# Optimization experiments

Hardware: AMD Instinct MI355X
Metric: run time of the kernel (lower is better)

## Reference

```python
import jax, jax.numpy as jnp
import numpy as np

N = 100000
IN_DIM = 256
H1 = 128
H2 = 64
E = 3200000


def setup_inputs() -> dict:
    key = jax.random.key(0)
    k1, k2, k3, k4 = jax.random.split(key, 4)
    x = jax.random.normal(k1, (N, IN_DIM), dtype=jnp.float32)
    edge_index = jax.random.randint(k2, (2, E), 0, N, dtype=jnp.int64)
    # GCNConv params (glorot weights, zero bias as in PyG defaults)
    W1 = jax.random.normal(k3, (IN_DIM, H1), dtype=jnp.float32) * (1.0 / np.sqrt(IN_DIM))
    b1 = jnp.zeros((H1,), dtype=jnp.float32)
    W2 = jax.random.normal(k4, (H1, H2), dtype=jnp.float32) * (1.0 / np.sqrt(H1))
    b2 = jnp.zeros((H2,), dtype=jnp.float32)
    return {"x": x, "edge_index": edge_index, "W1": W1, "b1": b1, "W2": W2, "b2": b2}


def _gcn_conv(x, W, b, row, col, norm, n_nodes):
    # PyG GCNConv: y = D^{-1/2} (A+I) D^{-1/2} (x W) + b
    h = x @ W                                   # [N, out]
    msg = h[col] * norm[:, None]                # gather + edge scaling
    agg = jax.ops.segment_sum(msg, row, num_segments=n_nodes)  # scatter-add
    return agg + b


def reference(x, edge_index, W1, b1, W2, b2):
    n_nodes = x.shape[0]
    # add self-loops
    loop = jnp.arange(n_nodes, dtype=edge_index.dtype)
    row = jnp.concatenate([edge_index[0], loop])  # target nodes
    col = jnp.concatenate([edge_index[1], loop])  # source nodes
    # symmetric normalization D^{-1/2} A_hat D^{-1/2}
    deg = jax.ops.segment_sum(jnp.ones_like(row, dtype=x.dtype), row, num_segments=n_nodes)
    dinv = jnp.where(deg > 0, jax.lax.rsqrt(deg), 0.0)
    norm = dinv[row] * dinv[col]                # per-edge coefficient
    h = jax.nn.relu(_gcn_conv(x, W1, b1, row, col, norm, n_nodes))
    z = jax.nn.relu(_gcn_conv(h, W2, b2, row, col, norm, n_nodes))
    return z
```

## Files before the change

### kernel.cpp

```cpp
#include <hip/hip_runtime.h>

constexpr int NN = 100000;
constexpr int NE = 3200000;
constexpr int D0 = 256;
constexpr int D1 = 128;
constexpr int D2 = 64;

constexpr int BSHIFT = 9;
constexpr int NPB = 1 << BSHIFT;
constexpr int NBUCK = (NN + NPB - 1) >> BSHIFT;
constexpr int PBLK = 256;
constexpr int CHUNK = (NE + PBLK - 1) / PBLK;

typedef unsigned short ushort8v __attribute__((ext_vector_type(8)));

static __device__ __forceinline__ float bf2f(unsigned short u) {
  return __uint_as_float(((unsigned)u) << 16);
}
static __device__ __forceinline__ unsigned short f2bf(float x) {
  unsigned u = __float_as_uint(x);
  unsigned r = (u + 0x7FFFu + ((u >> 16) & 1u)) >> 16;
  return (unsigned short)r;
}

__global__ __launch_bounds__(256) void count_bucket_k(const int* __restrict__ rows,
                                                      unsigned* __restrict__ gcnt) {
  __shared__ unsigned hist[NBUCK];
  int tid = threadIdx.x;
  for (int i = tid; i < NBUCK; i += 256) hist[i] = 0;
  __syncthreads();
  int s = blockIdx.x * CHUNK;
  int e = s + CHUNK; if (e > NE) e = NE;
  for (int i = s + tid; i < e; i += 256)
    atomicAdd(&hist[((unsigned)rows[i]) >> BSHIFT], 1u);
  __syncthreads();
  for (int i = tid; i < NBUCK; i += 256)
    if (hist[i]) atomicAdd(&gcnt[i], hist[i]);
}

__global__ __launch_bounds__(256) void bucket_scan_k(const unsigned* __restrict__ gcnt,
                                                     unsigned* __restrict__ boff,
                                                     unsigned* __restrict__ gcursor) {
  __shared__ unsigned s[256];
  int t = threadIdx.x;
  unsigned v = (t < NBUCK) ? gcnt[t] : 0u;
  s[t] = v;
  __syncthreads();
  for (int off = 1; off < 256; off <<= 1) {
    unsigned u = (t >= off) ? s[t - off] : 0u;
    __syncthreads();
    s[t] += u;
    __syncthreads();
  }
  if (t < NBUCK) {
    boff[t + 1] = s[t];
    gcursor[t] = s[t] - v;
  }
  if (t == 0) boff[0] = 0u;
}

__global__ __launch_bounds__(256) void partition_k(const int* __restrict__ rows,
                                                   const int* __restrict__ cols,
                                                   unsigned* __restrict__ gcursor,
                                                   unsigned* __restrict__ bucketed) {
  __shared__ unsigned hist[NBUCK], base[NBUCK];
  int tid = threadIdx.x;
  for (int i = tid; i < NBUCK; i += 256) hist[i] = 0;
  __syncthreads();
  int s = blockIdx.x * CHUNK;
  int e = s + CHUNK; if (e > NE) e = NE;
  for (int i = s + tid; i < e; i += 256)
    atomicAdd(&hist[((unsigned)rows[i]) >> BSHIFT], 1u);
  __syncthreads();
  for (int i = tid; i < NBUCK; i += 256)
    base[i] = hist[i] ? atomicAdd(&gcursor[i], hist[i]) : 0u;
  __syncthreads();
  for (int i = tid; i < NBUCK; i += 256) hist[i] = 0;
  __syncthreads();
  for (int i = s + tid; i < e; i += 256) {
    unsigned r = (unsigned)rows[i];
    unsigned b = r >> BSHIFT;
    unsigned p = ((r & (unsigned)(NPB - 1)) << 17) | (unsigned)cols[i];
    unsigned pos = base[b] + atomicAdd(&hist[b], 1u);
    bucketed[pos] = p;
  }
}

__global__ __launch_bounds__(256) void build_k(const unsigned* __restrict__ bucketed,
                                               const unsigned* __restrict__ boff,
                                               unsigned* __restrict__ row_start,
                                               float* __restrict__ dinv,
                                               int* __restrict__ col_sorted) {
  __shared__ unsigned hist[NPB], sc[NPB], cur[NPB];
  const int b = blockIdx.x, tid = threadIdx.x;
  hist[tid] = 0; hist[tid + 256] = 0;
  __syncthreads();
  const unsigned s0 = boff[b], e0 = boff[b + 1];
  for (unsigned i = s0 + tid; i < e0; i += 256)
    atomicAdd(&hist[bucketed[i] >> 17], 1u);
  __syncthreads();
  sc[tid] = hist[tid]; sc[tid + 256] = hist[tid + 256];
  __syncthreads();
  for (int off = 1; off < NPB; off <<= 1) {
    unsigned v0 = (tid >= off) ? sc[tid - off] : 0u;
    unsigned v1 = (tid + 256 >= off) ? sc[tid + 256 - off] : 0u;
    __syncthreads();
    sc[tid] += v0; sc[tid + 256] += v1;
    __syncthreads();
  }
  cur[tid] = tid ? sc[tid - 1] : 0u;
  cur[tid + 256] = sc[tid + 255];
  for (int idx = tid; idx <= NPB; idx += 256) {
    int node = b * NPB + idx;
    if (node <= NN) {
      unsigned ex = idx ? sc[idx - 1] : 0u;
      row_start[node] = s0 + ex;
      if (idx < NPB && node < NN) dinv[node] = rsqrtf((float)hist[idx] + 1.0f);
    }
  }
  __syncthreads();
  for (unsigned i = s0 + tid; i < e0; i += 256) {
    unsigned p = bucketed[i];
    unsigned pos = s0 + atomicAdd(&cur[p >> 17], 1u);
    col_sorted[pos] = (int)(p & 0x1FFFFu);
  }
}

template <int BM, int BN, int BK, int TM, int TN, int K, bool BF16_OUT>
__global__ __launch_bounds__(256) void gemm_scale_k(const float* __restrict__ A,
                                                    const float* __restrict__ W,
                                                    const float* __restrict__ dinv,
                                                    void* __restrict__ outp, int M) {
  constexpr int TX = BN / TN;
  constexpr int TY = BM / TM;
  static_assert(TX * TY == 256, "thread shape");
  __shared__ float As[BK][BM];
  __shared__ float Ws[BK][BN];
  const int tid = threadIdx.x;
  const int tx = tid % TX, ty = tid / TX;
  const int rowBase = blockIdx.x * BM;

  float acc[TM][TN];
#pragma unroll
  for (int i = 0; i < TM; i++)
#pragma unroll
    for (int j = 0; j < TN; j++) acc[i][j] = 0.f;

  constexpr int AF4 = BM * BK / 4 / 256;
  constexpr int WF4 = BK * BN / 4 / 256;

  for (int k0 = 0; k0 < K; k0 += BK) {
#pragma unroll
    for (int q = 0; q < AF4; q++) {
      int f = tid + q * 256;
      int r = f / (BK / 4);
      int kk = (f % (BK / 4)) * 4;
      float4 v = make_float4(0.f, 0.f, 0.f, 0.f);
      int gr = rowBase + r;
      if (gr < M) v = *(const float4*)&A[(size_t)gr * K + k0 + kk];
      As[kk + 0][r] = v.x;
      As[kk + 1][r] = v.y;
      As[kk + 2][r] = v.z;
      As[kk + 3][r] = v.w;
    }
#pragma unroll
    for (int q = 0; q < WF4; q++) {
      int f = tid + q * 256;
      int kk = f / (BN / 4);
      int c = (f % (BN / 4)) * 4;
      *(float4*)&Ws[kk][c] = *(const float4*)&W[(size_t)(k0 + kk) * BN + c];
    }
    __syncthreads();
#pragma unroll
    for (int kk = 0; kk < BK; kk++) {
      float a[TM], wv[TN];
#pragma unroll
      for (int i = 0; i < TM; i += 4) {
        float4 t = *(const float4*)&As[kk][ty * TM + i];
        a[i] = t.x; a[i + 1] = t.y; a[i + 2] = t.z; a[i + 3] = t.w;
      }
#pragma unroll
      for (int j = 0; j < TN; j += 4) {
        float4 t = *(const float4*)&Ws[kk][tx * TN + j];
        wv[j] = t.x; wv[j + 1] = t.y; wv[j + 2] = t.z; wv[j + 3] = t.w;
      }
#pragma unroll
      for (int i = 0; i < TM; i++)
#pragma unroll
        for (int j = 0; j < TN; j++) acc[i][j] += a[i] * wv[j];
    }
    __syncthreads();
  }

#pragma unroll
  for (int i = 0; i < TM; i++) {
    int gr = rowBase + ty * TM + i;
    if (gr < M) {
      float d = dinv[gr];
      if constexpr (BF16_OUT) {
        unsigned short* out = (unsigned short*)outp;
#pragma unroll
        for (int j = 0; j < TN; j += 4) {
          ushort4 o;
          o.x = f2bf(acc[i][j + 0] * d);
          o.y = f2bf(acc[i][j + 1] * d);
          o.z = f2bf(acc[i][j + 2] * d);
          o.w = f2bf(acc[i][j + 3] * d);
          *(ushort4*)&out[(size_t)gr * BN + tx * TN + j] = o;
        }
      } else {
        float* out = (float*)outp;
#pragma unroll
        for (int j = 0; j < TN; j += 4) {
          float4 o;
          o.x = acc[i][j + 0] * d;
          o.y = acc[i][j + 1] * d;
          o.z = acc[i][j + 2] * d;
          o.w = acc[i][j + 3] * d;
          *(float4*)&out[(size_t)gr * BN + tx * TN + j] = o;
        }
      }
    }
  }
}

__global__ __launch_bounds__(256) void prop1_k(const unsigned short* __restrict__ hp,
                                               const unsigned* __restrict__ row_start,
                                               const int* __restrict__ cols,
                                               const float* __restrict__ dinv,
                                               const float* __restrict__ bias,
                                               float* __restrict__ out) {
  int wid = (blockIdx.x * 256 + threadIdx.x) >> 6;
  int lane = threadIdx.x & 63;
  if (wid >= NN) return;
  const int r = wid;
  const int q = lane >> 4, f = lane & 15;

  float a0[8], a1[8];
#pragma unroll
  for (int k = 0; k < 8; k++) { a0[k] = 0.f; a1[k] = 0.f; }
  if (q == 0) {
    ushort8v v = *(const ushort8v*)(hp + (size_t)r * D1 + f * 8);
#pragma unroll
    for (int k = 0; k < 8; k++) a0[k] = bf2f(v[k]);
  }

  unsigned s = row_start[r], e = row_start[r + 1];
  for (unsigned base = s; base < e; base += 64) {
    int cnt = (int)min(64u, e - base);
    int c = (lane < cnt) ? cols[base + lane] : 0;
    int j = 0;
    for (; j + 8 <= cnt; j += 8) {
      int c0 = __shfl(c, j + q);
      int c1 = __shfl(c, j + 4 + q);
      ushort8v v0 = *(const ushort8v*)(hp + (size_t)c0 * D1 + f * 8);
      ushort8v v1 = *(const ushort8v*)(hp + (size_t)c1 * D1 + f * 8);
#pragma unroll
      for (int k = 0; k < 8; k++) a0[k] += bf2f(v0[k]);
#pragma unroll
      for (int k = 0; k < 8; k++) a1[k] += bf2f(v1[k]);
    }
    for (; j + 4 <= cnt; j += 4) {
      int c0 = __shfl(c, j + q);
      ushort8v v0 = *(const ushort8v*)(hp + (size_t)c0 * D1 + f * 8);
#pragma unroll
      for (int k = 0; k < 8; k++) a0[k] += bf2f(v0[k]);
    }
    if (j < cnt) {
      int c0 = __shfl(c, j + q);
      if (j + q < cnt) {
        ushort8v v0 = *(const ushort8v*)(hp + (size_t)c0 * D1 + f * 8);
#pragma unroll
        for (int k = 0; k < 8; k++) a0[k] += bf2f(v0[k]);
      }
    }
  }

#pragma unroll
  for (int k = 0; k < 8; k++) a0[k] += a1[k];
#pragma unroll
  for (int k = 0; k < 8; k++) a0[k] += __shfl_xor(a0[k], 16);
#pragma unroll
  for (int k = 0; k < 8; k++) a0[k] += __shfl_xor(a0[k], 32);

  if (q == 0) {
    float dr = dinv[r];
    float4 b0 = *(const float4*)&bias[f * 8];
    float4 b1v = *(const float4*)&bias[f * 8 + 4];
    float4 o0, o1;
    o0.x = fmaxf(a0[0] * dr + b0.x, 0.f);
    o0.y = fmaxf(a0[1] * dr + b0.y, 0.f);
    o0.z = fmaxf(a0[2] * dr + b0.z, 0.f);
    o0.w = fmaxf(a0[3] * dr + b0.w, 0.f);
    o1.x = fmaxf(a0[4] * dr + b1v.x, 0.f);
    o1.y = fmaxf(a0[5] * dr + b1v.y, 0.f);
    o1.z = fmaxf(a0[6] * dr + b1v.z, 0.f);
    o1.w = fmaxf(a0[7] * dr + b1v.w, 0.f);
    *(float4*)&out[(size_t)r * D1 + f * 8] = o0;
    *(float4*)&out[(size_t)r * D1 + f * 8 + 4] = o1;
  }
}

__global__ __launch_bounds__(256) void prop2_k(const unsigned short* __restrict__ hp,
                                               const unsigned* __restrict__ row_start,
                                               const int* __restrict__ cols,
                                               const float* __restrict__ dinv,
                                               const float* __restrict__ bias,
                                               float* __restrict__ out) {
  int wid = (blockIdx.x * 256 + threadIdx.x) >> 6;
  int lane = threadIdx.x & 63;
  if (wid >= NN) return;
  const int r = wid;
  const int q = lane >> 3, f = lane & 7;

  float a0[8], a1[8];
#pragma unroll
  for (int k = 0; k < 8; k++) { a0[k] = 0.f; a1[k] = 0.f; }
  if (q == 0) {
    ushort8v v = *(const ushort8v*)(hp + (size_t)r * D2 + f * 8);
#pragma unroll
    for (int k = 0; k < 8; k++) a0[k] = bf2f(v[k]);
  }

  unsigned s = row_start[r], e = row_start[r + 1];
  for (unsigned base = s; base < e; base += 64) {
    int cnt = (int)min(64u, e - base);
    int c = (lane < cnt) ? cols[base + lane] : 0;
    int j = 0;
    for (; j + 16 <= cnt; j += 16) {
      int c0 = __shfl(c, j + q);
      int c1 = __shfl(c, j + 8 + q);
      ushort8v v0 = *(const ushort8v*)(hp + (size_t)c0 * D2 + f * 8);
      ushort8v v1 = *(const ushort8v*)(hp + (size_t)c1 * D2 + f * 8);
#pragma unroll
      for (int k = 0; k < 8; k++) a0[k] += bf2f(v0[k]);
#pragma unroll
      for (int k = 0; k < 8; k++) a1[k] += bf2f(v1[k]);
    }
    for (; j + 8 <= cnt; j += 8) {
      int c0 = __shfl(c, j + q);
      ushort8v v0 = *(const ushort8v*)(hp + (size_t)c0 * D2 + f * 8);
#pragma unroll
      for (int k = 0; k < 8; k++) a0[k] += bf2f(v0[k]);
    }
    if (j < cnt) {
      int c0 = __shfl(c, j + q);
      if (j + q < cnt) {
        ushort8v v0 = *(const ushort8v*)(hp + (size_t)c0 * D2 + f * 8);
#pragma unroll
        for (int k = 0; k < 8; k++) a0[k] += bf2f(v0[k]);
      }
    }
  }

#pragma unroll
  for (int k = 0; k < 8; k++) a0[k] += a1[k];
#pragma unroll
  for (int k = 0; k < 8; k++) a0[k] += __shfl_xor(a0[k], 8);
#pragma unroll
  for (int k = 0; k < 8; k++) a0[k] += __shfl_xor(a0[k], 16);
#pragma unroll
  for (int k = 0; k < 8; k++) a0[k] += __shfl_xor(a0[k], 32);

  if (q == 0) {
    float dr = dinv[r];
    float4 b0 = *(const float4*)&bias[f * 8];
    float4 b1v = *(const float4*)&bias[f * 8 + 4];
    float4 o0, o1;
    o0.x = fmaxf(a0[0] * dr + b0.x, 0.f);
    o0.y = fmaxf(a0[1] * dr + b0.y, 0.f);
    o0.z = fmaxf(a0[2] * dr + b0.z, 0.f);
    o0.w = fmaxf(a0[3] * dr + b0.w, 0.f);
    o1.x = fmaxf(a0[4] * dr + b1v.x, 0.f);
    o1.y = fmaxf(a0[5] * dr + b1v.y, 0.f);
    o1.z = fmaxf(a0[6] * dr + b1v.z, 0.f);
    o1.w = fmaxf(a0[7] * dr + b1v.w, 0.f);
    *(float4*)&out[(size_t)r * D2 + f * 8] = o0;
    *(float4*)&out[(size_t)r * D2 + f * 8 + 4] = o1;
  }
}

extern "C" void kernel_launch(void* const* d_in, const int* in_sizes, int n_in,
                              void* d_out, int out_size, void* d_ws, size_t ws_size,
                              hipStream_t stream) {
  const float* x = (const float*)d_in[0];
  const int* ei = (const int*)d_in[1];
  const float* W1 = (const float*)d_in[2];
  const float* b1 = (const float*)d_in[3];
  const float* W2 = (const float*)d_in[4];
  const float* b2 = (const float*)d_in[5];
  float* z = (float*)d_out;

  const int* rows = ei;
  const int* cols = ei + NE;

  auto align_up = [](size_t v) { return (v + 511) & ~(size_t)511; };
  char* w = (char*)d_ws;
  unsigned* gcnt = (unsigned*)w;       w += align_up((size_t)NBUCK * 4);
  unsigned* boff = (unsigned*)w;       w += align_up((size_t)(NBUCK + 1) * 4);
  unsigned* gcursor = (unsigned*)w;    w += align_up((size_t)NBUCK * 4);
  unsigned* row_start = (unsigned*)w;  w += align_up((size_t)(NN + 1) * 4);
  float* dinv = (float*)w;             w += align_up((size_t)NN * 4);
  int* col_sorted = (int*)w;           w += align_up((size_t)NE * 4);
  unsigned short* hbf = (unsigned short*)w; w += align_up((size_t)NN * D1 * 2);
  float* h1 = (float*)w;               w += align_up((size_t)NN * D1 * 4);
  unsigned* bucketed = (unsigned*)h1;

  hipMemsetAsync(gcnt, 0, (size_t)NBUCK * 4, stream);

  count_bucket_k<<<PBLK, 256, 0, stream>>>(rows, gcnt);
  bucket_scan_k<<<1, 256, 0, stream>>>(gcnt, boff, gcursor);
  partition_k<<<PBLK, 256, 0, stream>>>(rows, cols, gcursor, bucketed);
  build_k<<<NBUCK, 256, 0, stream>>>(bucketed, boff, row_start, dinv, col_sorted);

  gemm_scale_k<64, 128, 32, 8, 4, 256, true>
      <<<(NN + 63) / 64, 256, 0, stream>>>(x, W1, dinv, hbf, NN);
  prop1_k<<<(NN + 3) / 4, 256, 0, stream>>>(hbf, row_start, col_sorted, dinv, b1, h1);

  gemm_scale_k<64, 64, 32, 4, 4, 128, true>
      <<<(NN + 63) / 64, 256, 0, stream>>>(h1, W2, dinv, hbf, NN);
  prop2_k<<<(NN + 3) / 4, 256, 0, stream>>>(hbf, row_start, col_sorted, dinv, b2, z);
}
```

Baseline: 537.5 us.

## Use bf16 MFMA for dense GEMMs and widen gather unroll in propagation

Replaces the FP32 scalar-FMA tiled GEMM with a bf16 MFMA kernel (16x16x32) that converts A and W tiles to bf16 in shared memory, with four waves each computing a quadrant of a 128-row tile. The propagation kernels also get a fourth-level unroll with four independent accumulator sets, so more neighbour gathers are in flight per wave. The goal is to cut GEMM compute time and hide gather latency. In exchange, inputs lose precision by rounding to bf16 before the multiply, the W tile is loaded with strided scalar reads, and the new epilogue writes scattered 2-byte stores.

```diff
diff --git a/kernel.cpp b/kernel.cpp
--- a/kernel.cpp
+++ b/kernel.cpp
@@ -13,6 +13,8 @@
 constexpr int CHUNK = (NE + PBLK - 1) / PBLK;
 
 typedef unsigned short ushort8v __attribute__((ext_vector_type(8)));
+typedef short short8v __attribute__((ext_vector_type(8)));
+typedef float float4v __attribute__((ext_vector_type(4)));
 
 static __device__ __forceinline__ float bf2f(unsigned short u) {
   return __uint_as_float(((unsigned)u) << 16);
@@ -126,98 +128,82 @@
   }
 }
 
-template <int BM, int BN, int BK, int TM, int TN, int K, bool BF16_OUT>
-__global__ __launch_bounds__(256) void gemm_scale_k(const float* __restrict__ A,
-                                                    const float* __restrict__ W,
-                                                    const float* __restrict__ dinv,
-                                                    void* __restrict__ outp, int M) {
-  constexpr int TX = BN / TN;
-  constexpr int TY = BM / TM;
-  static_assert(TX * TY == 256, "thread shape");
-  __shared__ float As[BK][BM];
-  __shared__ float Ws[BK][BN];
+template <int BM, int BN, int K>
+__global__ __launch_bounds__(256) void mfma_gemm_k(const float* __restrict__ A,
+                                                   const float* __restrict__ W,
+                                                   const float* __restrict__ dinv,
+                                                   unsigned short* __restrict__ out,
+                                                   int M) {
+  constexpr int MR = BM / 2 / 16;
+  constexpr int NR = BN / 2 / 16;
+  __shared__ __align__(16) unsigned short As[BM * 32];
+  __shared__ __align__(16) unsigned short Ws[BN * 32];
   const int tid = threadIdx.x;
-  const int tx = tid % TX, ty = tid / TX;
+  const int lane = tid & 63;
+  const int wid = tid >> 6;
+  const int wr = (wid >> 1) * (BM / 2);
+  const int wc = (wid & 1) * (BN / 2);
   const int rowBase = blockIdx.x * BM;
 
-  float acc[TM][TN];
-#pragma unroll
-  for (int i = 0; i < TM; i++)
-#pragma unroll
-    for (int j = 0; j < TN; j++) acc[i][j] = 0.f;
-
-  constexpr int AF4 = BM * BK / 4 / 256;
-  constexpr int WF4 = BK * BN / 4 / 256;
-
-  for (int k0 = 0; k0 < K; k0 += BK) {
-#pragma unroll
-    for (int q = 0; q < AF4; q++) {
-      int f = tid + q * 256;
-      int r = f / (BK / 4);
-      int kk = (f % (BK / 4)) * 4;
+  float4v acc[MR][NR];
+#pragma unroll
+  for (int i = 0; i < MR; i++)
+#pragma unroll
+    for (int j = 0; j < NR; j++) acc[i][j] = (float4v)0.f;
+
+  const int lr = lane & 15;
+  const int lk = (lane >> 4) << 3;
+
+  for (int k0 = 0; k0 < K; k0 += 32) {
+#pragma unroll
+    for (int g = tid; g < BM * 8; g += 256) {
+      int row = g >> 3, kg = g & 7;
+      int grow = rowBase + row;
       float4 v = make_float4(0.f, 0.f, 0.f, 0.f);
-      int gr = rowBase + r;
-      if (gr < M) v = *(const float4*)&A[(size_t)gr * K + k0 + kk];
-      As[kk + 0][r] = v.x;
-      As[kk + 1][r] = v.y;
-      As[kk + 2][r] = v.z;
-      As[kk + 3][r] = v.w;
-    }
-#pragma unroll
-    for (int q = 0; q < WF4; q++) {
-      int f = tid + q * 256;
-      int kk = f / (BN / 4);
-      int c = (f % (BN / 4)) * 4;
-      *(float4*)&Ws[kk][c] = *(const float4*)&W[(size_t)(k0 + kk) * BN + c];
-    }
-    __syncthreads();
-#pragma unroll
-    for (int kk = 0; kk < BK; kk++) {
-      float a[TM], wv[TN];
-#pragma unroll
-      for (int i = 0; i < TM; i += 4) {
-        float4 t = *(const float4*)&As[kk][ty * TM + i];
-        a[i] = t.x; a[i + 1] = t.y; a[i + 2] = t.z; a[i + 3] = t.w;
-      }
-#pragma unroll
-      for (int j = 0; j < TN; j += 4) {
-        float4 t = *(const float4*)&Ws[kk][tx * TN + j];
-        wv[j] = t.x; wv[j + 1] = t.y; wv[j + 2] = t.z; wv[j + 3] = t.w;
-      }
-#pragma unroll
-      for (int i = 0; i < TM; i++)
-#pragma unroll
-        for (int j = 0; j < TN; j++) acc[i][j] += a[i] * wv[j];
-    }
-    __syncthreads();
-  }
-
-#pragma unroll
-  for (int i = 0; i < TM; i++) {
-    int gr = rowBase + ty * TM + i;
-    if (gr < M) {
-      float d = dinv[gr];
-      if constexpr (BF16_OUT) {
-        unsigned short* out = (unsigned short*)outp;
-#pragma unroll
-        for (int j = 0; j < TN; j += 4) {
-          ushort4 o;
-          o.x = f2bf(acc[i][j + 0] * d);
-          o.y = f2bf(acc[i][j + 1] * d);
-          o.z = f2bf(acc[i][j + 2] * d);
-          o.w = f2bf(acc[i][j + 3] * d);
-          *(ushort4*)&out[(size_t)gr * BN + tx * TN + j] = o;
-        }
-      } else {
-        float* out = (float*)outp;
-#pragma unroll
-        for (int j = 0; j < TN; j += 4) {
-          float4 o;
-          o.x = acc[i][j + 0] * d;
-          o.y = acc[i][j + 1] * d;
-          o.z = acc[i][j + 2] * d;
-          o.w = acc[i][j + 3] * d;
-          *(float4*)&out[(size_t)gr * BN + tx * TN + j] = o;
+      if (grow < M) v = *(const float4*)&A[(size_t)grow * K + k0 + kg * 4];
+      ushort4 u;
+      u.x = f2bf(v.x); u.y = f2bf(v.y); u.z = f2bf(v.z); u.w = f2bf(v.w);
+      *(ushort4*)&As[row * 32 + kg * 4] = u;
+    }
+#pragma unroll
+    for (int g = tid; g < BN * 8; g += 256) {
+      int col = g % BN, kg = g / BN;
+      int k = k0 + kg * 4;
+      ushort4 u;
+      u.x = f2bf(W[(size_t)(k + 0) * BN + col]);
+      u.y = f2bf(W[(size_t)(k + 1) * BN + col]);
+      u.z = f2bf(W[(size_t)(k + 2) * BN + col]);
+      u.w = f2bf(W[(size_t)(k + 3) * BN + col]);
+      *(ushort4*)&Ws[col * 32 + kg * 4] = u;
+    }
+    __syncthreads();
+
+    short8v a[MR], b[NR];
+#pragma unroll
+    for (int mi = 0; mi < MR; mi++)
+      a[mi] = *(const short8v*)&As[(wr + mi * 16 + lr) * 32 + lk];
+#pragma unroll
+    for (int ni = 0; ni < NR; ni++)
+      b[ni] = *(const short8v*)&Ws[(wc + ni * 16 + lr) * 32 + lk];
+#pragma unroll
+    for (int mi = 0; mi < MR; mi++)
+#pragma unroll
+      for (int ni = 0; ni < NR; ni++)
+        acc[mi][ni] = __builtin_amdgcn_mfma_f32_16x16x32_bf16(a[mi], b[ni], acc[mi][ni], 0, 0, 0);
+    __syncthreads();
+  }
+
+#pragma unroll
+  for (int mi = 0; mi < MR; mi++) {
+#pragma unroll
+    for (int r = 0; r < 4; r++) {
+      int grow = rowBase + wr + mi * 16 + (lane >> 4) * 4 + r;
+      if (grow < M) {
+        float dv = dinv[grow];
+#pragma unroll
+        for (int ni = 0; ni < NR; ni++) {
+          int gcol = wc + ni * 16 + lr;
+          out[(size_t)grow * BN + gcol] = f2bf(acc[mi][ni][r] * dv);
         }
       }
     }
@@ -236,9 +222,9 @@
   const int r = wid;
   const int q = lane >> 4, f = lane & 15;
 
-  float a0[8], a1[8];
-#pragma unroll
-  for (int k = 0; k < 8; k++) { a0[k] = 0.f; a1[k] = 0.f; }
+  float a0[8], a1[8], a2[8], a3[8];
+#pragma unroll
+  for (int k = 0; k < 8; k++) { a0[k] = 0.f; a1[k] = 0.f; a2[k] = 0.f; a3[k] = 0.f; }
   if (q == 0) {
     ushort8v v = *(const ushort8v*)(hp + (size_t)r * D1 + f * 8);
 #pragma unroll
@@ -250,9 +236,24 @@
     int cnt = (int)min(64u, e - base);
     int c = (lane < cnt) ? cols[base + lane] : 0;
     int j = 0;
+    for (; j + 16 <= cnt; j += 16) {
+      int c0 = __shfl(c, j + q), c1 = __shfl(c, j + 4 + q);
+      int c2 = __shfl(c, j + 8 + q), c3 = __shfl(c, j + 12 + q);
+      ushort8v v0 = *(const ushort8v*)(hp + (size_t)c0 * D1 + f * 8);
+      ushort8v v1 = *(const ushort8v*)(hp + (size_t)c1 * D1 + f * 8);
+      ushort8v v2 = *(const ushort8v*)(hp + (size_t)c2 * D1 + f * 8);
+      ushort8v v3 = *(const ushort8v*)(hp + (size_t)c3 * D1 + f * 8);
+#pragma unroll
+      for (int k = 0; k < 8; k++) a0[k] += bf2f(v0[k]);
+#pragma unroll
+      for (int k = 0; k < 8; k++) a1[k] += bf2f(v1[k]);
+#pragma unroll
+      for (int k = 0; k < 8; k++) a2[k] += bf2f(v2[k]);
+#pragma unroll
+      for (int k = 0; k < 8; k++) a3[k] += bf2f(v3[k]);
+    }
     for (; j + 8 <= cnt; j += 8) {
-      int c0 = __shfl(c, j + q);
-      int c1 = __shfl(c, j + 4 + q);
+      int c0 = __shfl(c, j + q), c1 = __shfl(c, j + 4 + q);
       ushort8v v0 = *(const ushort8v*)(hp + (size_t)c0 * D1 + f * 8);
       ushort8v v1 = *(const ushort8v*)(hp + (size_t)c1 * D1 + f * 8);
 #pragma unroll
@@ -277,7 +278,7 @@
   }
 
 #pragma unroll
-  for (int k = 0; k < 8; k++) a0[k] += a1[k];
+  for (int k = 0; k < 8; k++) a0[k] += a1[k] + a2[k] + a3[k];
 #pragma unroll
   for (int k = 0; k < 8; k++) a0[k] += __shfl_xor(a0[k], 16);
 #pragma unroll
@@ -313,9 +314,9 @@
   const int r = wid;
   const int q = lane >> 3, f = lane & 7;
 
-  float a0[8], a1[8];
-#pragma unroll
-  for (int k = 0; k < 8; k++) { a0[k] = 0.f; a1[k] = 0.f; }
+  float a0[8], a1[8], a2[8], a3[8];
+#pragma unroll
+  for (int k = 0; k < 8; k++) { a0[k] = 0.f; a1[k] = 0.f; a2[k] = 0.f; a3[k] = 0.f; }
   if (q == 0) {
     ushort8v v = *(const ushort8v*)(hp + (size_t)r * D2 + f * 8);
 #pragma unroll
@@ -327,9 +328,24 @@
     int cnt = (int)min(64u, e - base);
     int c = (lane < cnt) ? cols[base + lane] : 0;
     int j = 0;
+    for (; j + 32 <= cnt; j += 32) {
+      int c0 = __shfl(c, j + q), c1 = __shfl(c, j + 8 + q);
+      int c2 = __shfl(c, j + 16 + q), c3 = __shfl(c, j + 24 + q);
+      ushort8v v0 = *(const ushort8v*)(hp + (size_t)c0 * D2 + f * 8);
+      ushort8v v1 = *(const ushort8v*)(hp + (size_t)c1 * D2 + f * 8);
+      ushort8v v2 = *(const ushort8v*)(hp + (size_t)c2 * D2 + f * 8);
+      ushort8v v3 = *(const ushort8v*)(hp + (size_t)c3 * D2 + f * 8);
+#pragma unroll
+      for (int k = 0; k < 8; k++) a0[k] += bf2f(v0[k]);
+#pragma unroll
+      for (int k = 0; k < 8; k++) a1[k] += bf2f(v1[k]);
+#pragma unroll
+      for (int k = 0; k < 8; k++) a2[k] += bf2f(v2[k]);
+#pragma unroll
+      for (int k = 0; k < 8; k++) a3[k] += bf2f(v3[k]);
+    }
     for (; j + 16 <= cnt; j += 16) {
-      int c0 = __shfl(c, j + q);
-      int c1 = __shfl(c, j + 8 + q);
+      int c0 = __shfl(c, j + q), c1 = __shfl(c, j + 8 + q);
       ushort8v v0 = *(const ushort8v*)(hp + (size_t)c0 * D2 + f * 8);
       ushort8v v1 = *(const ushort8v*)(hp + (size_t)c1 * D2 + f * 8);
 #pragma unroll
@@ -354,7 +370,7 @@
   }
 
 #pragma unroll
-  for (int k = 0; k < 8; k++) a0[k] += a1[k];
+  for (int k = 0; k < 8; k++) a0[k] += a1[k] + a2[k] + a3[k];
 #pragma unroll
   for (int k = 0; k < 8; k++) a0[k] += __shfl_xor(a0[k], 8);
 #pragma unroll
@@ -413,11 +429,11 @@
   partition_k<<<PBLK, 256, 0, stream>>>(rows, cols, gcursor, bucketed);
   build_k<<<NBUCK, 256, 0, stream>>>(bucketed, boff, row_start, dinv, col_sorted);
 
-  gemm_scale_k<64, 128, 32, 8, 4, 256, true>
-      <<<(NN + 63) / 64, 256, 0, stream>>>(x, W1, dinv, hbf, NN);
+  mfma_gemm_k<128, 128, 256>
+      <<<(NN + 127) / 128, 256, 0, stream>>>(x, W1, dinv, hbf, NN);
   prop1_k<<<(NN + 3) / 4, 256, 0, stream>>>(hbf, row_start, col_sorted, dinv, b1, h1);
 
-  gemm_scale_k<64, 64, 32, 4, 4, 128, true>
-      <<<(NN + 63) / 64, 256, 0, stream>>>(h1, W2, dinv, hbf, NN);
+  mfma_gemm_k<128, 64, 128>
+      <<<(NN + 127) / 128, 256, 0, stream>>>(h1, W2, dinv, hbf, NN);
   prop2_k<<<(NN + 3) / 4, 256, 0, stream>>>(hbf, row_start, col_sorted, dinv, b2, z);
 }
```

Measured after the change: 531.0 us. About the same (-1.2%).
